# Optimization experiments

Measured on AMD Instinct MI355X. Metric: run time of the kernel, lower is better.

The kernel has to match this reference:

```python
import jax, jax.numpy as jnp
import numpy as np

HEADS = 20
HEAD_DIM = 64
IP_WEIGHT = 1.0

def _sdpa(q, k, v):
    # q: [b,h,sq,d], k/v: [b,h,skv,d]
    scale = 1.0 / np.sqrt(q.shape[-1])
    logits = jnp.einsum('bhqd,bhkd->bhqk', q, k) * scale
    probs = jax.nn.softmax(logits, axis=-1)
    return jnp.einsum('bhqk,bhkd->bhqd', probs, v)

def _split_heads(t, b, h, d):
    return t.reshape(b, -1, h, d).transpose(0, 2, 1, 3)

def setup_inputs() -> dict:
    key = jax.random.key(0)
    ks = jax.random.split(key, 10)
    B, S, D, C, T = 4, 4096, 1280, 2048, 16
    def w(k, fan_in, shape):
        return jax.random.normal(k, shape, dtype=jnp.float32) / np.sqrt(fan_in)
    return {
        'x': jax.random.normal(ks[0], (B, S, D), dtype=jnp.float32),
        'context': jax.random.normal(ks[1], (B, 77, C), dtype=jnp.float32),
        'image_emb': jax.random.normal(ks[2], (B, T, C), dtype=jnp.float32),
        'Wq': w(ks[3], D, (D, D)),
        'Wk': w(ks[4], C, (C, D)),
        'Wv': w(ks[5], C, (C, D)),
        'Wk_ip': w(ks[6], C, (C, D)),
        'Wv_ip': w(ks[7], C, (C, D)),
        'Wo': w(ks[8], D, (D, D)),
        'bo': jnp.zeros((D,), dtype=jnp.float32),
    }

def reference(x, context, image_emb, Wq, Wk, Wv, Wk_ip, Wv_ip, Wo, bo):
    b, s, inner = x.shape
    h, d = HEADS, HEAD_DIM
    q = _split_heads(x @ Wq, b, h, d)            # [b,h,s,d]
    k = _split_heads(context @ Wk, b, h, d)      # [b,h,77,d]
    v = _split_heads(context @ Wv, b, h, d)
    out = _sdpa(q, k, v)                         # main cross-attn
    ip_k = _split_heads(image_emb @ Wk_ip, b, h, d)  # [b,h,16,d]
    ip_v = _split_heads(image_emb @ Wv_ip, b, h, d)
    ip_out = _sdpa(q, ip_k, ip_v)                # image-conditioned attn, same q
    out = out + IP_WEIGHT * ip_out
    out = out.transpose(0, 2, 1, 3).reshape(b, s, h * d)
    return out @ Wo + bo
```

## Files before the change

### kernel.cpp

```cpp
#include <hip/hip_runtime.h>
#include <cstdint>

typedef __bf16 bf16;
typedef __bf16 bf16x8 __attribute__((ext_vector_type(8)));
typedef float f32x4 __attribute__((ext_vector_type(4)));

#define MFMA16(a, b, c) __builtin_amdgcn_mfma_f32_16x16x32_bf16((a), (b), (c), 0, 0, 0)
#define GLDS16(g, l)                                                         \
  __builtin_amdgcn_global_load_lds(                                          \
      (__attribute__((address_space(1))) void*)(g),                          \
      (__attribute__((address_space(3))) void*)(l), 16, 0, 0)

__global__ void prep_all(const float* __restrict__ Wq, const float* __restrict__ Wo,
                         const float* __restrict__ Wk, const float* __restrict__ Wv,
                         const float* __restrict__ Wkip, const float* __restrict__ Wvip,
                         bf16* __restrict__ WqT, bf16* __restrict__ WoT,
                         bf16* __restrict__ WkT, bf16* __restrict__ WvT,
                         bf16* __restrict__ WkipT, bf16* __restrict__ WvipT,
                         const float* __restrict__ x, bf16* __restrict__ xb,
                         const float* __restrict__ ctx, bf16* __restrict__ ctxb,
                         const float* __restrict__ img, bf16* __restrict__ imgb) {
  const int z = blockIdx.z;
  const int tx = threadIdx.x, ty = threadIdx.y;
  if (z < 6) {
    const float* src = (z == 0) ? Wq : (z == 1) ? Wo : (z == 2) ? Wk
                      : (z == 3) ? Wv : (z == 4) ? Wkip : Wvip;
    bf16* dst = (z == 0) ? WqT : (z == 1) ? WoT : (z == 2) ? WkT
               : (z == 3) ? WvT : (z == 4) ? WkipT : WvipT;
    const int K = (z < 2) ? 1280 : 2048;
    const int N = 1280;
    __shared__ float t[32][33];
    const int bx = blockIdx.x * 32, by = blockIdx.y * 32;
    if (by >= K) return;
#pragma unroll
    for (int i = 0; i < 32; i += 8)
      t[ty + i][tx] = src[(long)(by + ty + i) * N + bx + tx];
    __syncthreads();
#pragma unroll
    for (int i = 0; i < 32; i += 8)
      dst[(long)(bx + ty + i) * K + by + tx] = (bf16)t[tx][ty + i];
    return;
  }
  const int tid = ty * 32 + tx;
  const int bid = blockIdx.y * 40 + blockIdx.x;
  const float* s;
  bf16* d;
  long base;
  if (z < 10) {
    base = (((long)(z - 6) * 2560 + bid) * 256 + tid) * 8;
    s = x; d = xb;
  } else if (bid < 308) {
    base = ((long)bid * 256 + tid) * 8;
    s = ctx; d = ctxb;
  } else if (bid < 372) {
    base = ((long)(bid - 308) * 256 + tid) * 8;
    s = img; d = imgb;
  } else {
    return;
  }
  float4 a = *(const float4*)(s + base);
  float4 b = *(const float4*)(s + base + 4);
  bf16x8 o;
  o[0] = (bf16)a.x; o[1] = (bf16)a.y; o[2] = (bf16)a.z; o[3] = (bf16)a.w;
  o[4] = (bf16)b.x; o[5] = (bf16)b.y; o[6] = (bf16)b.z; o[7] = (bf16)b.w;
  *(bf16x8*)(d + base) = o;
}

template <bool OUT_BF16, bool HAS_BIAS>
__device__ __forceinline__ void gemm256_core(const bf16* A, const bf16* Bt,
                                             void* Cp, const float* bias,
                                             int K, int N, int tm, int tn,
                                             int Mlim) {
  __shared__ bf16 Al[2][16384];
  __shared__ bf16 Bl[2][16384];
  const int tid = threadIdx.x;
  const int wave = tid >> 6, lane = tid & 63;
  const int g = lane >> 4, l16 = lane & 15;
  const int wr = wave >> 2, wc = wave & 3;

  const int srow = wave * 16 + (lane >> 3);
  const int scol = ((lane & 7) ^ ((lane >> 3) & 7)) * 8;
  const bf16* gA = A + (long)(tm + srow) * K + scol;
  const bf16* gB = Bt + (long)(tn + srow) * K + scol;
  const int ldst = wave * 1024;

#define STAGE_HALF(Lb_, gp_, b_, hh_, t_)                         \
  {                                                               \
    const bf16* s_ = (gp_) + (long)(hh_) * 128 * K + (t_) * 64;   \
    GLDS16(s_, &Lb_[b_][(hh_)*8192 + ldst]);                      \
    GLDS16(s_ + 8 * K, &Lb_[b_][(hh_)*8192 + ldst + 512]);        \
  }

  const int cs0 = (g ^ (l16 & 7)) * 8;
  const int cs1 = ((4 + g) ^ (l16 & 7)) * 8;
  const int aB0 = (wr * 64 + l16) * 64;
  const int aB1 = aB0 + 8192;
  const int bB = (wc * 64 + l16) * 64;

  f32x4 acc[8][4] = {};
  bf16x8 aF[4][2], bF[4][2];

  const int NT = K >> 6;

  STAGE_HALF(Al, gA, 0, 0, 0);
  STAGE_HALF(Al, gA, 0, 1, 0);
  STAGE_HALF(Bl, gB, 0, 0, 0);
  STAGE_HALF(Bl, gB, 0, 1, 0);
  STAGE_HALF(Al, gA, 1, 0, 1);
  STAGE_HALF(Bl, gB, 1, 0, 1);
  STAGE_HALF(Bl, gB, 1, 1, 1);
  asm volatile("s_waitcnt vmcnt(6)" ::: "memory");
  asm volatile("s_barrier" ::: "memory");

  for (int t = 0; t < NT; ++t) {
    const int b = t & 1;
#pragma unroll
    for (int mi = 0; mi < 4; ++mi) {
      aF[mi][0] = *(const bf16x8*)&Al[b][aB0 + mi * 1024 + cs0];
      aF[mi][1] = *(const bf16x8*)&Al[b][aB0 + mi * 1024 + cs1];
    }
#pragma unroll
    for (int nj = 0; nj < 2; ++nj) {
      bF[nj][0] = *(const bf16x8*)&Bl[b][bB + nj * 1024 + cs0];
      bF[nj][1] = *(const bf16x8*)&Bl[b][bB + nj * 1024 + cs1];
    }
    if (t + 1 < NT) STAGE_HALF(Al, gA, b ^ 1, 1, t + 1);
    asm volatile("s_barrier" ::: "memory");
    asm volatile("s_waitcnt lgkmcnt(0)" ::: "memory");
    __builtin_amdgcn_sched_barrier(0);
    __builtin_amdgcn_s_setprio(1);
#pragma unroll
    for (int mi = 0; mi < 4; ++mi)
#pragma unroll
      for (int nj = 0; nj < 2; ++nj) {
        acc[mi][nj] = MFMA16(aF[mi][0], bF[nj][0], acc[mi][nj]);
        acc[mi][nj] = MFMA16(aF[mi][1], bF[nj][1], acc[mi][nj]);
      }
    __builtin_amdgcn_s_setprio(0);
    asm volatile("s_barrier" ::: "memory");
#pragma unroll
    for (int nj = 2; nj < 4; ++nj) {
      bF[nj][0] = *(const bf16x8*)&Bl[b][bB + nj * 1024 + cs0];
      bF[nj][1] = *(const bf16x8*)&Bl[b][bB + nj * 1024 + cs1];
    }
    if (t + 2 < NT) STAGE_HALF(Al, gA, b, 0, t + 2);
    asm volatile("s_barrier" ::: "memory");
    asm volatile("s_waitcnt lgkmcnt(0)" ::: "memory");
    __builtin_amdgcn_sched_barrier(0);
    __builtin_amdgcn_s_setprio(1);
#pragma unroll
    for (int mi = 0; mi < 4; ++mi)
#pragma unroll
      for (int nj = 2; nj < 4; ++nj) {
        acc[mi][nj] = MFMA16(aF[mi][0], bF[nj][0], acc[mi][nj]);
        acc[mi][nj] = MFMA16(aF[mi][1], bF[nj][1], acc[mi][nj]);
      }
    __builtin_amdgcn_s_setprio(0);
    asm volatile("s_barrier" ::: "memory");
#pragma unroll
    for (int mi = 0; mi < 4; ++mi) {
      aF[mi][0] = *(const bf16x8*)&Al[b][aB1 + mi * 1024 + cs0];
      aF[mi][1] = *(const bf16x8*)&Al[b][aB1 + mi * 1024 + cs1];
    }
    if (t + 2 < NT) STAGE_HALF(Bl, gB, b, 0, t + 2);
    asm volatile("s_barrier" ::: "memory");
    asm volatile("s_waitcnt lgkmcnt(0)" ::: "memory");
    __builtin_amdgcn_sched_barrier(0);
    __builtin_amdgcn_s_setprio(1);
#pragma unroll
    for (int mi = 0; mi < 4; ++mi)
#pragma unroll
      for (int nj = 2; nj < 4; ++nj) {
        acc[4 + mi][nj] = MFMA16(aF[mi][0], bF[nj][0], acc[4 + mi][nj]);
        acc[4 + mi][nj] = MFMA16(aF[mi][1], bF[nj][1], acc[4 + mi][nj]);
      }
    __builtin_amdgcn_s_setprio(0);
    asm volatile("s_barrier" ::: "memory");
    if (t + 2 < NT) STAGE_HALF(Bl, gB, b, 1, t + 2);
    asm volatile("s_barrier" ::: "memory");
    __builtin_amdgcn_sched_barrier(0);
    __builtin_amdgcn_s_setprio(1);
#pragma unroll
    for (int mi = 0; mi < 4; ++mi)
#pragma unroll
      for (int nj = 0; nj < 2; ++nj) {
        acc[4 + mi][nj] = MFMA16(aF[mi][0], bF[nj][0], acc[4 + mi][nj]);
        acc[4 + mi][nj] = MFMA16(aF[mi][1], bF[nj][1], acc[4 + mi][nj]);
      }
    __builtin_amdgcn_s_setprio(0);
    if (t + 2 < NT) {
      asm volatile("s_waitcnt vmcnt(6)" ::: "memory");
    } else if (t + 1 < NT) {
      asm volatile("s_waitcnt vmcnt(0)" ::: "memory");
    }
    asm volatile("s_barrier" ::: "memory");
  }
#undef STAGE_HALF

#pragma unroll
  for (int mi = 0; mi < 8; ++mi) {
    const int rb = (mi < 4) ? (wr * 64 + mi * 16) : (128 + wr * 64 + (mi - 4) * 16);
#pragma unroll
    for (int nj = 0; nj < 4; ++nj) {
      const int col = tn + wc * 64 + nj * 16 + l16;
      float bv = 0.f;
      if (HAS_BIAS) bv = bias[col];
#pragma unroll
      for (int r = 0; r < 4; ++r) {
        const long row = (long)tm + rb + g * 4 + r;
        if (row < Mlim) {
          float v = acc[mi][nj][r] + bv;
          if (OUT_BF16)
            ((bf16*)Cp)[row * N + col] = (bf16)v;
          else
            ((float*)Cp)[row * N + col] = v;
        }
      }
    }
  }
}

__global__ __launch_bounds__(512, 2) void gemm_qproj_small(
    const bf16* __restrict__ xb, const bf16* __restrict__ WqT,
    bf16* __restrict__ qb, const bf16* __restrict__ ctxb,
    const bf16* __restrict__ imgb, const bf16* __restrict__ WkT,
    const bf16* __restrict__ WvT, const bf16* __restrict__ WkipT,
    const bf16* __restrict__ WvipT, bf16* __restrict__ kb,
    bf16* __restrict__ vb, bf16* __restrict__ ipkb, bf16* __restrict__ ipvb) {
  const int i = blockIdx.x;
  const bf16 *A, *Bt;
  bf16* C;
  int K, tm, tn, Mlim;
  if (i >= 30) {
    const int q = i - 30;
    const int local = q >> 3;
    A = xb; Bt = WqT; C = qb; K = 1280; Mlim = 1 << 30;
    tm = ((q & 7) * 8 + local / 5) * 256;
    tn = (local % 5) * 256;
  } else {
    int z, bx, by;
    if (i < 20) {
      z = i / 10;
      const int r = i % 10;
      bx = r / 5; by = r % 5;
    } else {
      z = 2 + (i - 20) / 5;
      bx = 0; by = (i - 20) % 5;
    }
    A = (z < 2) ? ctxb : imgb;
    Bt = (z == 0) ? WkT : (z == 1) ? WvT : (z == 2) ? WkipT : WvipT;
    C = (z == 0) ? kb : (z == 1) ? vb : (z == 2) ? ipkb : ipvb;
    K = 2048;
    tm = bx * 256;
    tn = by * 256;
    Mlim = (z < 2) ? 384 : 128;
  }
  gemm256_core<true, false>(A, Bt, C, nullptr, K, 1280, tm, tn, Mlim);
}

__global__ __launch_bounds__(512, 2) void gemm_f32out_bias(
    const bf16* __restrict__ A, const bf16* __restrict__ Bt,
    float* __restrict__ C, const float* __restrict__ bias, int K, int N) {
  const int i = blockIdx.x;
  const int local = i >> 3;
  const int tm = ((i & 7) * 8 + local / 5) * 256;
  const int tn = (local % 5) * 256;
  gemm256_core<false, true>(A, Bt, C, bias, K, N, tm, tn, 1 << 30);
}

__global__ __launch_bounds__(256) void attention_kernel(
    const bf16* __restrict__ q, const bf16* __restrict__ k,
    const bf16* __restrict__ v, const bf16* __restrict__ ipk,
    const bf16* __restrict__ ipv, bf16* __restrict__ out) {
  __shared__ bf16 Kl[96 * 64];
  __shared__ bf16 Vt[64 * 104];
  __shared__ bf16 Pl[4][16 * 104];

  const int b = blockIdx.z, h = blockIdx.y, qblk = blockIdx.x;
  const int tid = threadIdx.x;

  {
    uint32_t* vz = (uint32_t*)Vt;
    for (int i = tid; i < 64 * 104 / 2; i += 256) vz[i] = 0;
  }
  __syncthreads();

  for (int c = tid; c < 77 * 8; c += 256) {
    const int row = c >> 3, d0 = (c & 7) * 8;
    const long src = (long)(b * 77 + row) * 1280 + h * 64 + d0;
    bf16x8 kk = *(const bf16x8*)&k[src];
    *(bf16x8*)&Kl[row * 64 + (d0 ^ ((row & 7) << 3))] = kk;
    bf16x8 vv = *(const bf16x8*)&v[src];
#pragma unroll
    for (int i2 = 0; i2 < 8; i2++) Vt[(d0 + i2) * 104 + row] = vv[i2];
  }
  if (tid < 16 * 8) {
    const int r = tid >> 3, d0 = (tid & 7) * 8;
    const int row = 80 + r;
    const long src = (long)(b * 16 + r) * 1280 + h * 64 + d0;
    bf16x8 kk = *(const bf16x8*)&ipk[src];
    *(bf16x8*)&Kl[row * 64 + (d0 ^ ((row & 7) << 3))] = kk;
    bf16x8 vv = *(const bf16x8*)&ipv[src];
#pragma unroll
    for (int i2 = 0; i2 < 8; i2++) Vt[(d0 + i2) * 104 + row] = vv[i2];
  }
  __syncthreads();

  const int wave = tid >> 6, lane = tid & 63;
  const int g = lane >> 4, l16 = lane & 15;
  const float sc = 0.125f * 1.44269504f;

  for (int it = 0; it < 2; it++) {
    const long qrow = (long)b * 4096 + qblk * 128 + wave * 32 + it * 16;
    bf16x8 qf[2];
#pragma unroll
    for (int ks = 0; ks < 2; ks++)
      qf[ks] = *(const bf16x8*)&q[(qrow + l16) * 1280 + h * 64 + ks * 32 + g * 8];

    f32x4 lt[6];
#pragma unroll
    for (int t = 0; t < 6; t++) {
      f32x4 a = {0.f, 0.f, 0.f, 0.f};
#pragma unroll
      for (int ks = 0; ks < 2; ks++) {
        const int row = t * 16 + l16;
        const int d = (ks * 32 + g * 8) ^ ((row & 7) << 3);
        bf16x8 kb8 = *(const bf16x8*)&Kl[row * 64 + d];
        a = MFMA16(qf[ks], kb8, a);
      }
      lt[t] = a;
    }

    float p[6][4];
#pragma unroll
    for (int r = 0; r < 4; r++) {
      float lv[5], m = -3e38f;
#pragma unroll
      for (int t = 0; t < 5; t++) {
        const int kv = t * 16 + l16;
        lv[t] = (kv < 77) ? lt[t][r] * sc : -3e38f;
        m = fmaxf(m, lv[t]);
      }
      for (int msk = 1; msk < 16; msk <<= 1) m = fmaxf(m, __shfl_xor(m, msk, 16));
      float s = 0.f;
#pragma unroll
      for (int t = 0; t < 5; t++) {
        const float pp = exp2f(lv[t] - m);
        p[t][r] = pp;
        s += pp;
      }
      for (int msk = 1; msk < 16; msk <<= 1) s += __shfl_xor(s, msk, 16);
      const float inv = 1.f / s;
#pragma unroll
      for (int t = 0; t < 5; t++) p[t][r] *= inv;
      const float l5 = lt[5][r] * sc;
      float m2 = l5;
      for (int msk = 1; msk < 16; msk <<= 1) m2 = fmaxf(m2, __shfl_xor(m2, msk, 16));
      const float p5 = exp2f(l5 - m2);
      float s2 = p5;
      for (int msk = 1; msk < 16; msk <<= 1) s2 += __shfl_xor(s2, msk, 16);
      p[5][r] = p5 / s2;
    }

#pragma unroll
    for (int t = 0; t < 6; t++)
#pragma unroll
      for (int r = 0; r < 4; r++)
        Pl[wave][(g * 4 + r) * 104 + t * 16 + l16] = (bf16)p[t][r];
    __syncthreads();

    bf16x8 paf[3];
#pragma unroll
    for (int ks = 0; ks < 3; ks++)
      paf[ks] = *(const bf16x8*)&Pl[wave][l16 * 104 + ks * 32 + g * 8];
#pragma unroll
    for (int n = 0; n < 4; n++) {
      f32x4 o = {0.f, 0.f, 0.f, 0.f};
#pragma unroll
      for (int ks = 0; ks < 3; ks++) {
        bf16x8 vbf = *(const bf16x8*)&Vt[(n * 16 + l16) * 104 + ks * 32 + g * 8];
        o = MFMA16(paf[ks], vbf, o);
      }
#pragma unroll
      for (int r = 0; r < 4; r++)
        out[(qrow + g * 4 + r) * 1280 + h * 64 + n * 16 + l16] = (bf16)o[r];
    }
    __syncthreads();
  }
}

extern "C" void kernel_launch(void* const* d_in, const int* in_sizes, int n_in,
                              void* d_out, int out_size, void* d_ws,
                              size_t ws_size, hipStream_t stream) {
  const float* x = (const float*)d_in[0];
  const float* ctx = (const float*)d_in[1];
  const float* img = (const float*)d_in[2];
  const float* Wq = (const float*)d_in[3];
  const float* Wk = (const float*)d_in[4];
  const float* Wv = (const float*)d_in[5];
  const float* Wkip = (const float*)d_in[6];
  const float* Wvip = (const float*)d_in[7];
  const float* Wo = (const float*)d_in[8];
  const float* bo = (const float*)d_in[9];
  float* out = (float*)d_out;

  bf16* ws = (bf16*)d_ws;
  size_t o = 0;
  auto alloc = [&](size_t n) { bf16* p = ws + o; o += n; return p; };
  bf16* xattn = alloc(16384L * 1280);
  bf16* qb    = alloc(16384L * 1280);
  bf16* WqT   = alloc(1280L * 1280);
  bf16* WoT   = alloc(1280L * 1280);
  bf16* WkT   = alloc(1280L * 2048);
  bf16* WvT   = alloc(1280L * 2048);
  bf16* WkipT = alloc(1280L * 2048);
  bf16* WvipT = alloc(1280L * 2048);
  bf16* ctxb  = alloc(384L * 2048);
  bf16* imgb  = alloc(128L * 2048);
  bf16* kb    = alloc(384L * 1280);
  bf16* vb    = alloc(384L * 1280);
  bf16* ipkb  = alloc(128L * 1280);
  bf16* ipvb  = alloc(128L * 1280);

  prep_all<<<dim3(40, 64, 11), dim3(32, 8), 0, stream>>>(
      Wq, Wo, Wk, Wv, Wkip, Wvip, WqT, WoT, WkT, WvT, WkipT, WvipT, x, xattn,
      ctx, ctxb, img, imgb);

  gemm_qproj_small<<<350, 512, 0, stream>>>(xattn, WqT, qb, ctxb, imgb, WkT,
                                            WvT, WkipT, WvipT, kb, vb, ipkb,
                                            ipvb);

  attention_kernel<<<dim3(32, 20, 4), 256, 0, stream>>>(qb, kb, vb, ipkb, ipvb,
                                                        xattn);

  gemm_f32out_bias<<<320, 512, 0, stream>>>(xattn, WoT, out, bo, 1280, 1280);
}
```

Before: 264.3 us.

## Rework GEMM core into 4-stage BK=32 pipeline with register double-buffered fragments

Replaces the two-buffer BK=64 main loop, which had many barriers per iteration, with a four-slot LDS ring of BK=32 tiles, prefetched three tiles ahead. LDS fragments are double-buffered in registers, so the next tile's reads overlap the current MFMAs, and each iteration needs only one barrier. The warp row mapping changes so that each wave owns 128 contiguous rows. This aims to cut synchronisation stalls and hide load latency, at the cost of more register pressure and a K loop unrolled by two, which assumes K/32 is even.

```diff
diff --git a/kernel.cpp b/kernel.cpp
--- a/kernel.cpp
+++ b/kernel.cpp
@@ -71,135 +71,104 @@
                                              void* Cp, const float* bias,
                                              int K, int N, int tm, int tn,
                                              int Mlim) {
-  __shared__ bf16 Al[2][16384];
-  __shared__ bf16 Bl[2][16384];
+  __shared__ bf16 Al[4][256 * 32];
+  __shared__ bf16 Bl[4][256 * 32];
   const int tid = threadIdx.x;
   const int wave = tid >> 6, lane = tid & 63;
   const int g = lane >> 4, l16 = lane & 15;
   const int wr = wave >> 2, wc = wave & 3;
 
-  const int srow = wave * 16 + (lane >> 3);
-  const int scol = ((lane & 7) ^ ((lane >> 3) & 7)) * 8;
-  const bf16* gA = A + (long)(tm + srow) * K + scol;
-  const bf16* gB = Bt + (long)(tn + srow) * K + scol;
-  const int ldst = wave * 1024;
-
-#define STAGE_HALF(Lb_, gp_, b_, hh_, t_)                         \
-  {                                                               \
-    const bf16* s_ = (gp_) + (long)(hh_) * 128 * K + (t_) * 64;   \
-    GLDS16(s_, &Lb_[b_][(hh_)*8192 + ldst]);                      \
-    GLDS16(s_ + 8 * K, &Lb_[b_][(hh_)*8192 + ldst + 512]);        \
-  }
-
-  const int cs0 = (g ^ (l16 & 7)) * 8;
-  const int cs1 = ((4 + g) ^ (l16 & 7)) * 8;
-  const int aB0 = (wr * 64 + l16) * 64;
-  const int aB1 = aB0 + 8192;
-  const int bB = (wc * 64 + l16) * 64;
+  const int sr = lane >> 2;
+  const int sc = ((lane & 3) ^ ((lane >> 3) & 3)) * 8;
+  const bf16* ga0 = A + (long)(tm + wave * 16 + sr) * K + sc;
+  const bf16* ga1 = ga0 + (long)128 * K;
+  const bf16* gb0 = Bt + (long)(tn + wave * 16 + sr) * K + sc;
+  const bf16* gb1 = gb0 + (long)128 * K;
 
   f32x4 acc[8][4] = {};
-  bf16x8 aF[4][2], bF[4][2];
-
-  const int NT = K >> 6;
-
-  STAGE_HALF(Al, gA, 0, 0, 0);
-  STAGE_HALF(Al, gA, 0, 1, 0);
-  STAGE_HALF(Bl, gB, 0, 0, 0);
-  STAGE_HALF(Bl, gB, 0, 1, 0);
-  STAGE_HALF(Al, gA, 1, 0, 1);
-  STAGE_HALF(Bl, gB, 1, 0, 1);
-  STAGE_HALF(Bl, gB, 1, 1, 1);
-  asm volatile("s_waitcnt vmcnt(6)" ::: "memory");
+  const int rsw = (g ^ ((l16 >> 1) & 3)) * 8;
+  const int paOfs = (wr * 128 + l16) * 32 + rsw;
+  const int pbOfs = (wc * 64 + l16) * 32 + rsw;
+
+  const int NT = K >> 5;
+
+#define STAGE_TILE(t_, b_)                        \
+  {                                               \
+    const int kt_ = (t_) << 5;                    \
+    GLDS16(ga0 + kt_, &Al[b_][wave * 512]);       \
+    GLDS16(ga1 + kt_, &Al[b_][(wave + 8) * 512]); \
+    GLDS16(gb0 + kt_, &Bl[b_][wave * 512]);       \
+    GLDS16(gb1 + kt_, &Bl[b_][(wave + 8) * 512]); \
+  }
+
+  STAGE_TILE(0, 0);
+  STAGE_TILE(1, 1);
+  STAGE_TILE(2, 2);
+  asm volatile("s_waitcnt vmcnt(8)" ::: "memory");
   asm volatile("s_barrier" ::: "memory");
-
-  for (int t = 0; t < NT; ++t) {
-    const int b = t & 1;
-#pragma unroll
-    for (int mi = 0; mi < 4; ++mi) {
-      aF[mi][0] = *(const bf16x8*)&Al[b][aB0 + mi * 1024 + cs0];
-      aF[mi][1] = *(const bf16x8*)&Al[b][aB0 + mi * 1024 + cs1];
-    }
-#pragma unroll
-    for (int nj = 0; nj < 2; ++nj) {
-      bF[nj][0] = *(const bf16x8*)&Bl[b][bB + nj * 1024 + cs0];
-      bF[nj][1] = *(const bf16x8*)&Bl[b][bB + nj * 1024 + cs1];
-    }
-    if (t + 1 < NT) STAGE_HALF(Al, gA, b ^ 1, 1, t + 1);
-    asm volatile("s_barrier" ::: "memory");
-    asm volatile("s_waitcnt lgkmcnt(0)" ::: "memory");
-    __builtin_amdgcn_sched_barrier(0);
-    __builtin_amdgcn_s_setprio(1);
-#pragma unroll
-    for (int mi = 0; mi < 4; ++mi)
-#pragma unroll
-      for (int nj = 0; nj < 2; ++nj) {
-        acc[mi][nj] = MFMA16(aF[mi][0], bF[nj][0], acc[mi][nj]);
-        acc[mi][nj] = MFMA16(aF[mi][1], bF[nj][1], acc[mi][nj]);
-      }
-    __builtin_amdgcn_s_setprio(0);
-    asm volatile("s_barrier" ::: "memory");
-#pragma unroll
-    for (int nj = 2; nj < 4; ++nj) {
-      bF[nj][0] = *(const bf16x8*)&Bl[b][bB + nj * 1024 + cs0];
-      bF[nj][1] = *(const bf16x8*)&Bl[b][bB + nj * 1024 + cs1];
-    }
-    if (t + 2 < NT) STAGE_HALF(Al, gA, b, 0, t + 2);
-    asm volatile("s_barrier" ::: "memory");
-    asm volatile("s_waitcnt lgkmcnt(0)" ::: "memory");
-    __builtin_amdgcn_sched_barrier(0);
-    __builtin_amdgcn_s_setprio(1);
-#pragma unroll
-    for (int mi = 0; mi < 4; ++mi)
-#pragma unroll
-      for (int nj = 2; nj < 4; ++nj) {
-        acc[mi][nj] = MFMA16(aF[mi][0], bF[nj][0], acc[mi][nj]);
-        acc[mi][nj] = MFMA16(aF[mi][1], bF[nj][1], acc[mi][nj]);
-      }
-    __builtin_amdgcn_s_setprio(0);
-    asm volatile("s_barrier" ::: "memory");
-#pragma unroll
-    for (int mi = 0; mi < 4; ++mi) {
-      aF[mi][0] = *(const bf16x8*)&Al[b][aB1 + mi * 1024 + cs0];
-      aF[mi][1] = *(const bf16x8*)&Al[b][aB1 + mi * 1024 + cs1];
-    }
-    if (t + 2 < NT) STAGE_HALF(Bl, gB, b, 0, t + 2);
-    asm volatile("s_barrier" ::: "memory");
-    asm volatile("s_waitcnt lgkmcnt(0)" ::: "memory");
-    __builtin_amdgcn_sched_barrier(0);
-    __builtin_amdgcn_s_setprio(1);
-#pragma unroll
-    for (int mi = 0; mi < 4; ++mi)
-#pragma unroll
-      for (int nj = 2; nj < 4; ++nj) {
-        acc[4 + mi][nj] = MFMA16(aF[mi][0], bF[nj][0], acc[4 + mi][nj]);
-        acc[4 + mi][nj] = MFMA16(aF[mi][1], bF[nj][1], acc[4 + mi][nj]);
-      }
-    __builtin_amdgcn_s_setprio(0);
-    asm volatile("s_barrier" ::: "memory");
-    if (t + 2 < NT) STAGE_HALF(Bl, gB, b, 1, t + 2);
-    asm volatile("s_barrier" ::: "memory");
-    __builtin_amdgcn_sched_barrier(0);
-    __builtin_amdgcn_s_setprio(1);
-#pragma unroll
-    for (int mi = 0; mi < 4; ++mi)
-#pragma unroll
-      for (int nj = 0; nj < 2; ++nj) {
-        acc[4 + mi][nj] = MFMA16(aF[mi][0], bF[nj][0], acc[4 + mi][nj]);
-        acc[4 + mi][nj] = MFMA16(aF[mi][1], bF[nj][1], acc[4 + mi][nj]);
-      }
-    __builtin_amdgcn_s_setprio(0);
-    if (t + 2 < NT) {
-      asm volatile("s_waitcnt vmcnt(6)" ::: "memory");
-    } else if (t + 1 < NT) {
-      asm volatile("s_waitcnt vmcnt(0)" ::: "memory");
-    }
-    asm volatile("s_barrier" ::: "memory");
-  }
-#undef STAGE_HALF
+  bf16x8 a0[4], a1[4], a2[4], a3[4], b0[4], b1[4];
+  {
+    const bf16* pb_ = &Bl[0][pbOfs];
+#pragma unroll
+    for (int j = 0; j < 4; j++) b0[j] = *(const bf16x8*)(pb_ + j * 512);
+    const bf16* pa_ = &Al[0][paOfs];
+#pragma unroll
+    for (int i = 0; i < 4; i++) a0[i] = *(const bf16x8*)(pa_ + i * 512);
+#pragma unroll
+    for (int i = 0; i < 4; i++) a1[i] = *(const bf16x8*)(pa_ + 2048 + i * 512);
+  }
+  int slc = 0;
+
+#define GEMM_ITER(t_, aLoC, aHiC, bC, aLoN, aHiN, bN)                    \
+  {                                                                      \
+    asm volatile("s_waitcnt lgkmcnt(0)" ::: "memory");                   \
+    __builtin_amdgcn_sched_barrier(0);                                   \
+    if ((t_) + 3 < NT) {                                                 \
+      STAGE_TILE((t_) + 3, (slc + 3) & 3);                               \
+      asm volatile("s_waitcnt vmcnt(8)" ::: "memory");                   \
+    } else if ((t_) + 1 < NT) {                                          \
+      asm volatile("s_waitcnt vmcnt(0)" ::: "memory");                   \
+    }                                                                    \
+    asm volatile("s_barrier" ::: "memory");                              \
+    const int srd_ = (slc + 1) & 3;                                      \
+    if ((t_) + 1 < NT) {                                                 \
+      const bf16* pb_ = &Bl[srd_][pbOfs];                                \
+      _Pragma("unroll") for (int j_ = 0; j_ < 4; j_++)                   \
+          bN[j_] = *(const bf16x8*)(pb_ + j_ * 512);                     \
+      const bf16* pa_ = &Al[srd_][paOfs];                                \
+      _Pragma("unroll") for (int i_ = 0; i_ < 4; i_++)                   \
+          aLoN[i_] = *(const bf16x8*)(pa_ + i_ * 512);                   \
+    }                                                                    \
+    __builtin_amdgcn_sched_barrier(0);                                   \
+    __builtin_amdgcn_s_setprio(1);                                       \
+    _Pragma("unroll") for (int i_ = 0; i_ < 4; i_++)                     \
+        _Pragma("unroll") for (int j_ = 0; j_ < 4; j_++)                 \
+            acc[i_][j_] = MFMA16(aLoC[i_], bC[j_], acc[i_][j_]);         \
+    __builtin_amdgcn_s_setprio(0);                                       \
+    __builtin_amdgcn_sched_barrier(0);                                   \
+    if ((t_) + 1 < NT) {                                                 \
+      const bf16* pa_ = &Al[srd_][paOfs + 2048];                         \
+      _Pragma("unroll") for (int i_ = 0; i_ < 4; i_++)                   \
+          aHiN[i_] = *(const bf16x8*)(pa_ + i_ * 512);                   \
+    }                                                                    \
+    __builtin_amdgcn_sched_barrier(0);                                   \
+    __builtin_amdgcn_s_setprio(1);                                       \
+    _Pragma("unroll") for (int i_ = 0; i_ < 4; i_++)                     \
+        _Pragma("unroll") for (int j_ = 0; j_ < 4; j_++)                 \
+            acc[4 + i_][j_] = MFMA16(aHiC[i_], bC[j_], acc[4 + i_][j_]); \
+    __builtin_amdgcn_s_setprio(0);                                       \
+    slc = srd_;                                                          \
+  }
+
+  for (int t = 0; t < NT; t += 2) {
+    GEMM_ITER(t, a0, a1, b0, a2, a3, b1);
+    GEMM_ITER(t + 1, a2, a3, b1, a0, a1, b0);
+  }
+#undef GEMM_ITER
+#undef STAGE_TILE
 
 #pragma unroll
   for (int mi = 0; mi < 8; ++mi) {
-    const int rb = (mi < 4) ? (wr * 64 + mi * 16) : (128 + wr * 64 + (mi - 4) * 16);
 #pragma unroll
     for (int nj = 0; nj < 4; ++nj) {
       const int col = tn + wc * 64 + nj * 16 + l16;
@@ -207,7 +176,7 @@
       if (HAS_BIAS) bv = bias[col];
 #pragma unroll
       for (int r = 0; r < 4; ++r) {
-        const long row = (long)tm + rb + g * 4 + r;
+        const long row = (long)tm + wr * 128 + mi * 16 + g * 4 + r;
         if (row < Mlim) {
           float v = acc[mi][nj][r] + bv;
           if (OUT_BF16)
```

New measurement: 267.1 us. Within noise of the previous version (+1.0%).
